# Optimization experiments

Hardware: AMD Instinct MI355X
Metric: run time of the kernel (lower is better)

## Reference

```python
import jax, jax.numpy as jnp
import numpy as np

E = 1024  # embedding_size
H = 16    # multi_head_num


def setup_inputs() -> dict:
    key = jax.random.key(0)
    ks = jax.random.split(key, 9)
    B, N = 4, 1024
    s = 1.0 / np.sqrt(E)
    return {
        "x": jax.random.normal(ks[0], (B, N, E), dtype=jnp.float32),
        "Wq": jax.random.normal(ks[1], (E, E), dtype=jnp.float32) * s,
        "bq": jax.random.normal(ks[2], (E,), dtype=jnp.float32) * 0.02,
        "Wk": jax.random.normal(ks[3], (E, E), dtype=jnp.float32) * s,
        "bk": jax.random.normal(ks[4], (E,), dtype=jnp.float32) * 0.02,
        "Wv": jax.random.normal(ks[5], (E, E), dtype=jnp.float32) * s,
        "bv": jax.random.normal(ks[6], (E,), dtype=jnp.float32) * 0.02,
        "Wo": jax.random.normal(ks[7], (E, E), dtype=jnp.float32) * s,
        "bo": jax.random.normal(ks[8], (E,), dtype=jnp.float32) * 0.02,
    }


def reference(x, Wq, bq, Wk, bk, Wv, bv, Wo, bo):
    B, N, _ = x.shape
    d = E // H

    def heads(y):  # [B,N,E] -> [B,H,N,d]
        return y.reshape(B, N, H, d).transpose(0, 2, 1, 3)

    q = heads(x @ Wq.T + bq)
    k = heads(x @ Wk.T + bk)
    v = heads(x @ Wv.T + bv)

    energy = jnp.einsum('bhqd,bhkd->bhqk', q, k)
    # NOTE: module divides by sqrt(E) AFTER softmax (faithful to source)
    scaling = jnp.asarray(E, x.dtype) ** 0.5
    att = jax.nn.softmax(energy, axis=-1) / scaling
    out = jnp.einsum('bhal,bhlv->bhav', att, v)
    out = out.transpose(0, 2, 1, 3).reshape(B, N, E)
    return out @ Wo.T + bo
```

## Files before the change

### kernel.cpp

```cpp
#include <hip/hip_runtime.h>
#include <hip/hip_bf16.h>


typedef __bf16 bf16x8 __attribute__((ext_vector_type(8)));
typedef __bf16 bf16x4 __attribute__((ext_vector_type(4)));
typedef float  f32x4  __attribute__((ext_vector_type(4)));

__device__ __forceinline__ void glds16(const __bf16* g, __bf16* l) {
  __builtin_amdgcn_global_load_lds(
      (const __attribute__((address_space(1))) void*)g,
      (__attribute__((address_space(3))) void*)l, 16, 0, 0);
}

__global__ __launch_bounds__(256) void cvt_f32_bf16(const float* __restrict__ in,
                                                    __bf16* __restrict__ out, int n4) {
  int i = blockIdx.x * 256 + threadIdx.x;
  if (i < n4) {
    float4 v = *(const float4*)(in + (size_t)i * 4);
    bf16x4 b = {(__bf16)v.x, (__bf16)v.y, (__bf16)v.z, (__bf16)v.w};
    *(bf16x4*)(out + (size_t)i * 4) = b;
  }
}

__global__ __launch_bounds__(256) void cvt_all(const float* __restrict__ x,
                                               const float* __restrict__ Wq,
                                               const float* __restrict__ Wk,
                                               const float* __restrict__ Wv,
                                               const float* __restrict__ Wo,
                                               __bf16* __restrict__ xb,
                                               __bf16* __restrict__ Wqb,
                                               __bf16* __restrict__ Wkb,
                                               __bf16* __restrict__ Wvb,
                                               __bf16* __restrict__ Wob) {
  const int i = blockIdx.x * 256 + threadIdx.x;
  const float* src;
  __bf16* dst;
  int off;
  if (i < 1048576) {
    src = x; dst = xb; off = i;
  } else {
    const int j = i - 1048576;
    const int seg = j >> 18;
    off = j & 262143;
    src = (seg == 0) ? Wq : (seg == 1) ? Wk : (seg == 2) ? Wv : Wo;
    dst = (seg == 0) ? Wqb : (seg == 1) ? Wkb : (seg == 2) ? Wvb : Wob;
  }
  float4 v = *(const float4*)(src + (size_t)off * 4);
  bf16x4 b = {(__bf16)v.x, (__bf16)v.y, (__bf16)v.z, (__bf16)v.w};
  *(bf16x4*)(dst + (size_t)off * 4) = b;
}

template <bool WBF16>
__global__ __launch_bounds__(256) void gemm_qkv(const __bf16* __restrict__ A,
                                                const void* __restrict__ Wqp,
                                                const void* __restrict__ Wkp,
                                                const void* __restrict__ Wvp,
                                                const float* __restrict__ bq,
                                                const float* __restrict__ bk,
                                                const float* __restrict__ bv,
                                                __bf16* __restrict__ Qw,
                                                __bf16* __restrict__ Kw,
                                                __bf16* __restrict__ Vw) {
  constexpr int BST = WBF16 ? 64 : 72;
  __shared__ __attribute__((aligned(16))) __bf16 As[64][64];
  __shared__ __attribute__((aligned(16))) __bf16 Bs[128 * BST];

  const int tid = threadIdx.x;
  const int lane = tid & 63, w = tid >> 6;
  const int wm = w >> 1, wn = w & 1;
  const int l15 = lane & 15, lq = lane >> 4;
  const int lr = lane >> 3, lc = lane & 7;
  const int xs = l15 & 7;
  const int m0 = blockIdx.y * 64, n0 = blockIdx.x * 128;
  const int z = blockIdx.z;

  const void* Wp = (z == 0) ? Wqp : (z == 1) ? Wkp : Wvp;
  const float* bias = (z == 0) ? bq : (z == 1) ? bk : bv;
  __bf16* C = (z == 0) ? Qw : (z == 1) ? Kw : Vw;

  f32x4 acc[2][4] = {};

  for (int k0 = 0; k0 < 1024; k0 += 64) {
#pragma unroll
    for (int i = 0; i < 2; ++i) {
      const int row = w * 16 + i * 8 + lr;
      glds16(A + (size_t)(m0 + row) * 1024 + k0 + ((lc ^ lr) * 8), &As[row][lc * 8]);
    }
    if (WBF16) {
      const __bf16* Wb = (const __bf16*)Wp;
#pragma unroll
      for (int i = 0; i < 4; ++i) {
        const int row = w * 32 + i * 8 + lr;
        glds16(Wb + (size_t)(n0 + row) * 1024 + k0 + ((lc ^ lr) * 8), &Bs[row * 64 + lc * 8]);
      }
    } else {
      const float* W = (const float*)Wp;
#pragma unroll
      for (int i = 0; i < 8; ++i) {
        const int c = i * 256 + tid, row = c >> 4, col = (c & 15) * 4;
        float4 wv = *(const float4*)(W + (size_t)(n0 + row) * 1024 + k0 + col);
        bf16x4 b4 = {(__bf16)wv.x, (__bf16)wv.y, (__bf16)wv.z, (__bf16)wv.w};
        *(bf16x4*)(&Bs[row * 72 + col]) = b4;
      }
    }
    __syncthreads();
#pragma unroll
    for (int s = 0; s < 2; ++s) {
      bf16x8 af[2], bfv[4];
#pragma unroll
      for (int mt = 0; mt < 2; ++mt)
        af[mt] = *(const bf16x8*)(&As[wm * 32 + mt * 16 + l15][((s * 4 + lq) ^ xs) * 8]);
#pragma unroll
      for (int nt = 0; nt < 4; ++nt) {
        const int row = wn * 64 + nt * 16 + l15;
        if (WBF16)
          bfv[nt] = *(const bf16x8*)(&Bs[row * 64 + (((s * 4 + lq) ^ xs) * 8)]);
        else
          bfv[nt] = *(const bf16x8*)(&Bs[row * 72 + s * 32 + lq * 8]);
      }
#pragma unroll
      for (int mt = 0; mt < 2; ++mt)
#pragma unroll
        for (int nt = 0; nt < 4; ++nt)
          acc[mt][nt] = __builtin_amdgcn_mfma_f32_16x16x32_bf16(
              af[mt], bfv[nt], acc[mt][nt], 0, 0, 0);
    }
    __syncthreads();
  }

#pragma unroll
  for (int mt = 0; mt < 2; ++mt) {
    const int mg_base = m0 + wm * 32 + mt * 16 + lq * 4;
    const int b = mg_base >> 10, nr0 = mg_base & 1023;
#pragma unroll
    for (int nt = 0; nt < 4; ++nt) {
      const int ng = n0 + wn * 64 + nt * 16 + l15;
      const float bv = bias[ng];
      const int h = ng >> 6, dd = ng & 63;
      if (z != 2) {
#pragma unroll
        for (int r = 0; r < 4; ++r) {
          const int mg = mg_base + r;
          const size_t idx =
              ((size_t)(b * 16 + h) << 16) + (size_t)(mg & 1023) * 64 + dd;
          C[idx] = (__bf16)(acc[mt][nt][r] + bv);
        }
      } else {
        bf16x4 o4 = {(__bf16)(acc[mt][nt][0] + bv), (__bf16)(acc[mt][nt][1] + bv),
                     (__bf16)(acc[mt][nt][2] + bv), (__bf16)(acc[mt][nt][3] + bv)};
        *(bf16x4*)(&C[((size_t)(b * 16 + h) << 16) + (size_t)dd * 1024 + nr0]) = o4;
      }
    }
  }
}

__global__ __launch_bounds__(256) void gemm_out(const __bf16* __restrict__ A,
                                                const __bf16* __restrict__ W,
                                                const float* __restrict__ bias,
                                                float* __restrict__ C) {
  __shared__ __attribute__((aligned(16))) __bf16 As[64][64];
  __shared__ __attribute__((aligned(16))) __bf16 Bs[128][64];

  const int tid = threadIdx.x;
  const int lane = tid & 63, w = tid >> 6;
  const int wm = w >> 1, wn = w & 1;
  const int l15 = lane & 15, lq = lane >> 4;
  const int lr = lane >> 3, lc = lane & 7;
  const int xs = l15 & 7;
  const int m0 = blockIdx.y * 64, n0 = blockIdx.x * 128;

  f32x4 acc[2][4] = {};

  for (int k0 = 0; k0 < 1024; k0 += 64) {
#pragma unroll
    for (int i = 0; i < 2; ++i) {
      const int row = w * 16 + i * 8 + lr;
      glds16(A + (size_t)(m0 + row) * 1024 + k0 + ((lc ^ lr) * 8), &As[row][lc * 8]);
    }
#pragma unroll
    for (int i = 0; i < 4; ++i) {
      const int row = w * 32 + i * 8 + lr;
      glds16(W + (size_t)(n0 + row) * 1024 + k0 + ((lc ^ lr) * 8), &Bs[row][lc * 8]);
    }
    __syncthreads();
#pragma unroll
    for (int s = 0; s < 2; ++s) {
      bf16x8 af[2], bfv[4];
#pragma unroll
      for (int mt = 0; mt < 2; ++mt)
        af[mt] = *(const bf16x8*)(&As[wm * 32 + mt * 16 + l15][((s * 4 + lq) ^ xs) * 8]);
#pragma unroll
      for (int nt = 0; nt < 4; ++nt)
        bfv[nt] = *(const bf16x8*)(&Bs[wn * 64 + nt * 16 + l15][((s * 4 + lq) ^ xs) * 8]);
#pragma unroll
      for (int mt = 0; mt < 2; ++mt)
#pragma unroll
        for (int nt = 0; nt < 4; ++nt)
          acc[mt][nt] = __builtin_amdgcn_mfma_f32_16x16x32_bf16(
              af[mt], bfv[nt], acc[mt][nt], 0, 0, 0);
    }
    __syncthreads();
  }

#pragma unroll
  for (int mt = 0; mt < 2; ++mt) {
    const int mg_base = m0 + wm * 32 + mt * 16 + lq * 4;
#pragma unroll
    for (int nt = 0; nt < 4; ++nt) {
      const int ng = n0 + wn * 64 + nt * 16 + l15;
      const float bv = bias[ng];
#pragma unroll
      for (int r = 0; r < 4; ++r)
        C[(size_t)(mg_base + r) * 1024 + ng] = acc[mt][nt][r] + bv;
    }
  }
}

__global__ __launch_bounds__(256) void attn_kernel(const __bf16* __restrict__ Q,
                                                   const __bf16* __restrict__ K,
                                                   const __bf16* __restrict__ Vt,
                                                   __bf16* __restrict__ O) {
  __shared__ __attribute__((aligned(16))) __bf16 Qs[64][64];
  __shared__ __attribute__((aligned(16))) __bf16 Ks[64][64];
  __shared__ __attribute__((aligned(16))) __bf16 Vs[64][64];
  __shared__ __attribute__((aligned(16))) __bf16 Ps[4][16][72];

  const int tid = threadIdx.x;
  const int lane = tid & 63, w = tid >> 6;
  const int l15 = lane & 15, lq = lane >> 4;
  const int lr = lane >> 3, lc = lane & 7;
  const int xs = l15 & 7;

  const int qt = blockIdx.x;
  const int bh = blockIdx.y;
  const __bf16* Qh = Q + (size_t)bh * 65536;
  const __bf16* Kh = K + (size_t)bh * 65536;
  const __bf16* Vh = Vt + (size_t)bh * 65536;

#pragma unroll
  for (int i = 0; i < 2; ++i) {
    const int c = i * 256 + tid, row = c >> 3, c8 = c & 7;
    bf16x8 v = *(const bf16x8*)(Qh + (size_t)qt * 4096 + row * 64 + c8 * 8);
    *(bf16x8*)(&Qs[row][(c8 ^ (row & 7)) * 8]) = v;
  }

  float l_run = 0.0f;
  f32x4 oacc[4] = {};

  for (int kb = 0; kb < 16; ++kb) {
    __syncthreads();
#pragma unroll
    for (int i = 0; i < 2; ++i) {
      const int row = w * 16 + i * 8 + lr;
      glds16(Kh + (size_t)kb * 4096 + (size_t)row * 64 + ((lc ^ lr) * 8), &Ks[row][lc * 8]);
      glds16(Vh + (size_t)row * 1024 + kb * 64 + ((lc ^ lr) * 8), &Vs[row][lc * 8]);
    }
    __syncthreads();

    f32x4 sacc[4] = {};
#pragma unroll
    for (int s = 0; s < 2; ++s) {
      bf16x8 bq = *(const bf16x8*)(&Qs[w * 16 + l15][((s * 4 + lq) ^ xs) * 8]);
#pragma unroll
      for (int mt = 0; mt < 4; ++mt) {
        bf16x8 ak = *(const bf16x8*)(&Ks[mt * 16 + l15][((s * 4 + lq) ^ xs) * 8]);
        sacc[mt] = __builtin_amdgcn_mfma_f32_16x16x32_bf16(ak, bq, sacc[mt], 0, 0, 0);
      }
    }

    float sum = 0.0f;
#pragma unroll
    for (int mt = 0; mt < 4; ++mt)
#pragma unroll
      for (int r = 0; r < 4; ++r) {
        const float e = __expf(sacc[mt][r]);
        sacc[mt][r] = e;
        sum += e;
      }
    sum += __shfl_xor(sum, 16, 64);
    sum += __shfl_xor(sum, 32, 64);
    l_run += sum;

#pragma unroll
    for (int mt = 0; mt < 4; ++mt) {
      bf16x4 p4 = {(__bf16)sacc[mt][0], (__bf16)sacc[mt][1],
                   (__bf16)sacc[mt][2], (__bf16)sacc[mt][3]};
      *(bf16x4*)(&Ps[w][l15][mt * 16 + lq * 4]) = p4;
    }
    __threadfence_block();

#pragma unroll
    for (int s = 0; s < 2; ++s) {
      bf16x8 bp = *(const bf16x8*)(&Ps[w][l15][s * 32 + lq * 8]);
#pragma unroll
      for (int mt = 0; mt < 4; ++mt) {
        bf16x8 av = *(const bf16x8*)(&Vs[mt * 16 + l15][((s * 4 + lq) ^ xs) * 8]);
        oacc[mt] = __builtin_amdgcn_mfma_f32_16x16x32_bf16(av, bp, oacc[mt], 0, 0, 0);
      }
    }
  }

  const int b = bh >> 4, h = bh & 15;
  const float inv = 1.0f / (l_run * 32.0f);
  const size_t base = (size_t)(b * 1024 + qt * 64 + w * 16 + l15) * 1024 + h * 64;
#pragma unroll
  for (int mt = 0; mt < 4; ++mt) {
    bf16x4 o4 = {(__bf16)(oacc[mt][0] * inv), (__bf16)(oacc[mt][1] * inv),
                 (__bf16)(oacc[mt][2] * inv), (__bf16)(oacc[mt][3] * inv)};
    *(bf16x4*)(&O[base + mt * 16 + lq * 4]) = o4;
  }
}

extern "C" void kernel_launch(void* const* d_in, const int* in_sizes, int n_in,
                              void* d_out, int out_size, void* d_ws, size_t ws_size,
                              hipStream_t stream) {
  const float* x  = (const float*)d_in[0];
  const float* Wq = (const float*)d_in[1];
  const float* bq = (const float*)d_in[2];
  const float* Wk = (const float*)d_in[3];
  const float* bk = (const float*)d_in[4];
  const float* Wv = (const float*)d_in[5];
  const float* bv = (const float*)d_in[6];
  const float* Wo = (const float*)d_in[7];
  const float* bo = (const float*)d_in[8];
  float* out = (float*)d_out;

  const size_t SZ = (size_t)4 * 1024 * 1024;
  __bf16* Qw = (__bf16*)d_ws;
  __bf16* Kw = Qw + SZ;
  __bf16* Vw = Kw + SZ;
  __bf16* s3 = Vw + SZ;
  __bf16* xb = s3;
  __bf16* Ow = s3;

  dim3 blk(256);

  if (ws_size >= (size_t)40 * 1024 * 1024) {
    __bf16* Wqb = s3 + SZ;
    __bf16* Wkb = Wqb + SZ / 4;
    __bf16* Wvb = Wkb + SZ / 4;
    __bf16* Wob = Wvb + SZ / 4;
    cvt_all<<<8192, blk, 0, stream>>>(x, Wq, Wk, Wv, Wo, xb, Wqb, Wkb, Wvb, Wob);
    gemm_qkv<true><<<dim3(8, 64, 3), blk, 0, stream>>>(xb, Wqb, Wkb, Wvb,
                                                       bq, bk, bv, Qw, Kw, Vw);
    attn_kernel<<<dim3(16, 64), blk, 0, stream>>>(Qw, Kw, Vw, Ow);
    gemm_out<<<dim3(8, 64), blk, 0, stream>>>(Ow, Wob, bo, out);
  } else {
    __bf16* Wob = Kw;
    cvt_f32_bf16<<<4096, blk, 0, stream>>>(x, xb, 1048576);
    gemm_qkv<false><<<dim3(8, 64, 3), blk, 0, stream>>>(xb, Wq, Wk, Wv,
                                                        bq, bk, bv, Qw, Kw, Vw);
    attn_kernel<<<dim3(16, 64), blk, 0, stream>>>(Qw, Kw, Vw, Ow);
    cvt_f32_bf16<<<1024, blk, 0, stream>>>(Wo, Wob, 262144);
    gemm_out<<<dim3(8, 64), blk, 0, stream>>>(Ow, Wob, bo, out);
  }
}
```

Before: 177.9 us.

## Double attention query tile, fold log2e into Q, shrink out-proj tile

```diff
diff --git a/kernel.cpp b/kernel.cpp
--- a/kernel.cpp
+++ b/kernel.cpp
@@ -5,6 +5,8 @@
 typedef __bf16 bf16x8 __attribute__((ext_vector_type(8)));
 typedef __bf16 bf16x4 __attribute__((ext_vector_type(4)));
 typedef float  f32x4  __attribute__((ext_vector_type(4)));
+
+#define LOG2E 1.44269504f
 
 __device__ __forceinline__ void glds16(const __bf16* g, __bf16* l) {
   __builtin_amdgcn_global_load_lds(
@@ -77,6 +79,7 @@
   const void* Wp = (z == 0) ? Wqp : (z == 1) ? Wkp : Wvp;
   const float* bias = (z == 0) ? bq : (z == 1) ? bk : bv;
   __bf16* C = (z == 0) ? Qw : (z == 1) ? Kw : Vw;
+  const float scale = (z == 0) ? LOG2E : 1.0f;
 
   f32x4 acc[2][4] = {};
 
@@ -143,7 +146,7 @@
           const int mg = mg_base + r;
           const size_t idx =
               ((size_t)(b * 16 + h) << 16) + (size_t)(mg & 1023) * 64 + dd;
-          C[idx] = (__bf16)(acc[mt][nt][r] + bv);
+          C[idx] = (__bf16)((acc[mt][nt][r] + bv) * scale);
         }
       } else {
         bf16x4 o4 = {(__bf16)(acc[mt][nt][0] + bv), (__bf16)(acc[mt][nt][1] + bv),
@@ -159,7 +162,7 @@
                                                 const float* __restrict__ bias,
                                                 float* __restrict__ C) {
   __shared__ __attribute__((aligned(16))) __bf16 As[64][64];
-  __shared__ __attribute__((aligned(16))) __bf16 Bs[128][64];
+  __shared__ __attribute__((aligned(16))) __bf16 Bs[64][64];
 
   const int tid = threadIdx.x;
   const int lane = tid & 63, w = tid >> 6;
@@ -167,35 +170,31 @@
   const int l15 = lane & 15, lq = lane >> 4;
   const int lr = lane >> 3, lc = lane & 7;
   const int xs = l15 & 7;
-  const int m0 = blockIdx.y * 64, n0 = blockIdx.x * 128;
-
-  f32x4 acc[2][4] = {};
+  const int m0 = blockIdx.y * 64, n0 = blockIdx.x * 64;
+
+  f32x4 acc[2][2] = {};
 
   for (int k0 = 0; k0 < 1024; k0 += 64) {
 #pragma unroll
     for (int i = 0; i < 2; ++i) {
       const int row = w * 16 + i * 8 + lr;
       glds16(A + (size_t)(m0 + row) * 1024 + k0 + ((lc ^ lr) * 8), &As[row][lc * 8]);
-    }
-#pragma unroll
-    for (int i = 0; i < 4; ++i) {
-      const int row = w * 32 + i * 8 + lr;
       glds16(W + (size_t)(n0 + row) * 1024 + k0 + ((lc ^ lr) * 8), &Bs[row][lc * 8]);
     }
     __syncthreads();
 #pragma unroll
     for (int s = 0; s < 2; ++s) {
-      bf16x8 af[2], bfv[4];
+      bf16x8 af[2], bfv[2];
 #pragma unroll
       for (int mt = 0; mt < 2; ++mt)
         af[mt] = *(const bf16x8*)(&As[wm * 32 + mt * 16 + l15][((s * 4 + lq) ^ xs) * 8]);
 #pragma unroll
-      for (int nt = 0; nt < 4; ++nt)
-        bfv[nt] = *(const bf16x8*)(&Bs[wn * 64 + nt * 16 + l15][((s * 4 + lq) ^ xs) * 8]);
+      for (int nt = 0; nt < 2; ++nt)
+        bfv[nt] = *(const bf16x8*)(&Bs[wn * 32 + nt * 16 + l15][((s * 4 + lq) ^ xs) * 8]);
 #pragma unroll
       for (int mt = 0; mt < 2; ++mt)
 #pragma unroll
-        for (int nt = 0; nt < 4; ++nt)
+        for (int nt = 0; nt < 2; ++nt)
           acc[mt][nt] = __builtin_amdgcn_mfma_f32_16x16x32_bf16(
               af[mt], bfv[nt], acc[mt][nt], 0, 0, 0);
     }
@@ -206,8 +205,8 @@
   for (int mt = 0; mt < 2; ++mt) {
     const int mg_base = m0 + wm * 32 + mt * 16 + lq * 4;
 #pragma unroll
-    for (int nt = 0; nt < 4; ++nt) {
-      const int ng = n0 + wn * 64 + nt * 16 + l15;
+    for (int nt = 0; nt < 2; ++nt) {
+      const int ng = n0 + wn * 32 + nt * 16 + l15;
       const float bv = bias[ng];
 #pragma unroll
       for (int r = 0; r < 4; ++r)
@@ -220,10 +219,10 @@
                                                    const __bf16* __restrict__ K,
                                                    const __bf16* __restrict__ Vt,
                                                    __bf16* __restrict__ O) {
-  __shared__ __attribute__((aligned(16))) __bf16 Qs[64][64];
+  __shared__ __attribute__((aligned(16))) __bf16 Qs[128][64];
   __shared__ __attribute__((aligned(16))) __bf16 Ks[64][64];
   __shared__ __attribute__((aligned(16))) __bf16 Vs[64][64];
-  __shared__ __attribute__((aligned(16))) __bf16 Ps[4][16][72];
+  __shared__ __attribute__((aligned(16))) __bf16 Ps[4][2][16][72];
 
   const int tid = threadIdx.x;
   const int lane = tid & 63, w = tid >> 6;
@@ -238,14 +237,13 @@
   const __bf16* Vh = Vt + (size_t)bh * 65536;
 
 #pragma unroll
-  for (int i = 0; i < 2; ++i) {
-    const int c = i * 256 + tid, row = c >> 3, c8 = c & 7;
-    bf16x8 v = *(const bf16x8*)(Qh + (size_t)qt * 4096 + row * 64 + c8 * 8);
-    *(bf16x8*)(&Qs[row][(c8 ^ (row & 7)) * 8]) = v;
-  }
-
-  float l_run = 0.0f;
-  f32x4 oacc[4] = {};
+  for (int i = 0; i < 4; ++i) {
+    const int row = w * 32 + i * 8 + lr;
+    glds16(Qh + (size_t)(qt * 128 + row) * 64 + ((lc ^ lr) * 8), &Qs[row][lc * 8]);
+  }
+
+  float l_run[2] = {0.0f, 0.0f};
+  f32x4 oacc[2][4] = {};
 
   for (int kb = 0; kb < 16; ++kb) {
     __syncthreads();
@@ -257,57 +255,73 @@
     }
     __syncthreads();
 
-    f32x4 sacc[4] = {};
+    f32x4 sacc[2][4] = {};
 #pragma unroll
     for (int s = 0; s < 2; ++s) {
-      bf16x8 bq = *(const bf16x8*)(&Qs[w * 16 + l15][((s * 4 + lq) ^ xs) * 8]);
+      bf16x8 ak[4];
+#pragma unroll
+      for (int mt = 0; mt < 4; ++mt)
+        ak[mt] = *(const bf16x8*)(&Ks[mt * 16 + l15][((s * 4 + lq) ^ xs) * 8]);
+#pragma unroll
+      for (int g = 0; g < 2; ++g) {
+        bf16x8 bq = *(const bf16x8*)(&Qs[w * 32 + g * 16 + l15][((s * 4 + lq) ^ xs) * 8]);
+#pragma unroll
+        for (int mt = 0; mt < 4; ++mt)
+          sacc[g][mt] = __builtin_amdgcn_mfma_f32_16x16x32_bf16(ak[mt], bq, sacc[g][mt], 0, 0, 0);
+      }
+    }
+
+#pragma unroll
+    for (int g = 0; g < 2; ++g) {
+      float sum = 0.0f;
+#pragma unroll
+      for (int mt = 0; mt < 4; ++mt)
+#pragma unroll
+        for (int r = 0; r < 4; ++r) {
+          const float e = __builtin_amdgcn_exp2f(sacc[g][mt][r]);
+          sacc[g][mt][r] = e;
+          sum += e;
+        }
+      sum += __shfl_xor(sum, 16, 64);
+      sum += __shfl_xor(sum, 32, 64);
+      l_run[g] += sum;
 #pragma unroll
       for (int mt = 0; mt < 4; ++mt) {
-        bf16x8 ak = *(const bf16x8*)(&Ks[mt * 16 + l15][((s * 4 + lq) ^ xs) * 8]);
-        sacc[mt] = __builtin_amdgcn_mfma_f32_16x16x32_bf16(ak, bq, sacc[mt], 0, 0, 0);
-      }
-    }
-
-    float sum = 0.0f;
-#pragma unroll
-    for (int mt = 0; mt < 4; ++mt)
-#pragma unroll
-      for (int r = 0; r < 4; ++r) {
-        const float e = __expf(sacc[mt][r]);
-        sacc[mt][r] = e;
-        sum += e;
-      }
-    sum += __shfl_xor(sum, 16, 64);
-    sum += __shfl_xor(sum, 32, 64);
-    l_run += sum;
-
+        bf16x4 p4 = {(__bf16)sacc[g][mt][0], (__bf16)sacc[g][mt][1],
+                     (__bf16)sacc[g][mt][2], (__bf16)sacc[g][mt][3]};
+        *(bf16x4*)(&Ps[w][g][l15][mt * 16 + lq * 4]) = p4;
+      }
+    }
+    __threadfence_block();
+
+#pragma unroll
+    for (int s = 0; s < 2; ++s) {
+      bf16x8 av[4];
+#pragma unroll
+      for (int mt = 0; mt < 4; ++mt)
+        av[mt] = *(const bf16x8*)(&Vs[mt * 16 + l15][((s * 4 + lq) ^ xs) * 8]);
+#pragma unroll
+      for (int g = 0; g < 2; ++g) {
+        bf16x8 bp = *(const bf16x8*)(&Ps[w][g][l15][s * 32 + lq * 8]);
+#pragma unroll
+        for (int mt = 0; mt < 4; ++mt)
+          oacc[g][mt] = __builtin_amdgcn_mfma_f32_16x16x32_bf16(av[mt], bp, oacc[g][mt], 0, 0, 0);
+      }
+    }
+  }
+
+  const int b = bh >> 4, h = bh & 15;
+#pragma unroll
+  for (int g = 0; g < 2; ++g) {
+    const float inv = 1.0f / (l_run[g] * 32.0f);
+    const size_t base =
+        (size_t)(b * 1024 + qt * 128 + w * 32 + g * 16 + l15) * 1024 + h * 64;
 #pragma unroll
     for (int mt = 0; mt < 4; ++mt) {
-      bf16x4 p4 = {(__bf16)sacc[mt][0], (__bf16)sacc[mt][1],
-                   (__bf16)sacc[mt][2], (__bf16)sacc[mt][3]};
-      *(bf16x4*)(&Ps[w][l15][mt * 16 + lq * 4]) = p4;
-    }
-    __threadfence_block();
-
-#pragma unroll
-    for (int s = 0; s < 2; ++s) {
-      bf16x8 bp = *(const bf16x8*)(&Ps[w][l15][s * 32 + lq * 8]);
-#pragma unroll
-      for (int mt = 0; mt < 4; ++mt) {
-        bf16x8 av = *(const bf16x8*)(&Vs[mt * 16 + l15][((s * 4 + lq) ^ xs) * 8]);
-        oacc[mt] = __builtin_amdgcn_mfma_f32_16x16x32_bf16(av, bp, oacc[mt], 0, 0, 0);
-      }
-    }
-  }
-
-  const int b = bh >> 4, h = bh & 15;
-  const float inv = 1.0f / (l_run * 32.0f);
-  const size_t base = (size_t)(b * 1024 + qt * 64 + w * 16 + l15) * 1024 + h * 64;
-#pragma unroll
-  for (int mt = 0; mt < 4; ++mt) {
-    bf16x4 o4 = {(__bf16)(oacc[mt][0] * inv), (__bf16)(oacc[mt][1] * inv),
-                 (__bf16)(oacc[mt][2] * inv), (__bf16)(oacc[mt][3] * inv)};
-    *(bf16x4*)(&O[base + mt * 16 + lq * 4]) = o4;
+      bf16x4 o4 = {(__bf16)(oacc[g][mt][0] * inv), (__bf16)(oacc[g][mt][1] * inv),
+                   (__bf16)(oacc[g][mt][2] * inv), (__bf16)(oacc[g][mt][3] * inv)};
+      *(bf16x4*)(&O[base + mt * 16 + lq * 4]) = o4;
+    }
   }
 }
 
@@ -343,15 +357,15 @@
     cvt_all<<<8192, blk, 0, stream>>>(x, Wq, Wk, Wv, Wo, xb, Wqb, Wkb, Wvb, Wob);
     gemm_qkv<true><<<dim3(8, 64, 3), blk, 0, stream>>>(xb, Wqb, Wkb, Wvb,
                                                        bq, bk, bv, Qw, Kw, Vw);
-    attn_kernel<<<dim3(16, 64), blk, 0, stream>>>(Qw, Kw, Vw, Ow);
-    gemm_out<<<dim3(8, 64), blk, 0, stream>>>(Ow, Wob, bo, out);
+    attn_kernel<<<dim3(8, 64), blk, 0, stream>>>(Qw, Kw, Vw, Ow);
+    gemm_out<<<dim3(16, 64), blk, 0, stream>>>(Ow, Wob, bo, out);
   } else {
     __bf16* Wob = Kw;
     cvt_f32_bf16<<<4096, blk, 0, stream>>>(x, xb, 1048576);
     gemm_qkv<false><<<dim3(8, 64, 3), blk, 0, stream>>>(xb, Wq, Wk, Wv,
                                                         bq, bk, bv, Qw, Kw, Vw);
-    attn_kernel<<<dim3(16, 64), blk, 0, stream>>>(Qw, Kw, Vw, Ow);
+    attn_kernel<<<dim3(8, 64), blk, 0, stream>>>(Qw, Kw, Vw, Ow);
     cvt_f32_bf16<<<1024, blk, 0, stream>>>(Wo, Wob, 262144);
-    gemm_out<<<dim3(8, 64), blk, 0, stream>>>(Ow, Wob, bo, out);
-  }
-}
+    gemm_out<<<dim3(16, 64), blk, 0, stream>>>(Ow, Wob, bo, out);
+  }
+}
```

Measured after the change: 183.7 us. 1.03x slower.
